# Performance work log

Hardware: AMD Instinct MI355X
Metric: run time of the kernel (lower is better)

Reference implementation:

```python
import jax, jax.numpy as jnp
import numpy as np

N = 100000      # total sampled nodes
NT = 20000      # target (destination) nodes
E = 2000000     # edges
IN = 128        # in_dim
OUT = 64        # out_channels (heads=1, concat)
NEG_SLOPE = 0.2 # GATConv default negative_slope


def setup_inputs() -> dict:
    key = jax.random.key(0)
    ks = jax.random.split(key, 6)
    x = jax.random.normal(ks[0], (N, IN), dtype=jnp.float32)
    edge_src = jax.random.randint(ks[1], (E,), 0, N)
    edge_dst = jax.random.randint(ks[2], (E,), 0, NT)
    # GATConv params: shared lin for src/dst (in_channels is int), att vectors, bias
    W = jax.random.normal(ks[3], (IN, OUT), dtype=jnp.float32) / np.sqrt(IN).astype(np.float32)
    att_src = jax.random.normal(ks[4], (OUT,), dtype=jnp.float32)
    att_dst = jax.random.normal(ks[5], (OUT,), dtype=jnp.float32)
    bias = jnp.zeros((OUT,), dtype=jnp.float32)
    return {"x": x, "edge_src": edge_src, "edge_dst": edge_dst,
            "W": W, "att_src": att_src, "att_dst": att_dst, "bias": bias,
            "num_target": NT}


def reference(x, edge_src, edge_dst, W, att_src, att_dst, bias, num_target):
    # Linear transform (lin_src == lin_dst in PyG GATConv when in_channels is int)
    x_proj = x @ W                      # [N, OUT]
    x_dst = x_proj[:num_target]         # [NT, OUT] target nodes are x[:num_target]
    # Per-node attention logits
    a_src = x_proj @ att_src            # [N]
    a_dst = x_dst @ att_dst             # [NT]
    # Edge logits + LeakyReLU
    e = jax.nn.leaky_relu(a_src[edge_src] + a_dst[edge_dst], NEG_SLOPE)  # [E]
    # Segment softmax over edges grouped by destination
    m = jax.ops.segment_max(e, edge_dst, num_segments=num_target)
    m = jnp.where(jnp.isneginf(m), jnp.float32(0.0), m)  # empty segments
    p = jnp.exp(e - m[edge_dst])
    denom = jax.ops.segment_sum(p, edge_dst, num_segments=num_target)
    alpha = p / (denom[edge_dst] + jnp.float32(1e-16))   # PyG softmax eps
    # Weighted scatter-aggregate of source features
    out = jax.ops.segment_sum(alpha[:, None] * x_proj[edge_src], edge_dst,
                              num_segments=num_target)   # [NT, OUT]
    return out + bias
```

## Files before the change

kernel.cpp:

```cpp
#include <hip/hip_runtime.h>

#define IN_DIM 128
#define OUT_DIM 64
#define NEG_SLOPE 0.2f

#define NBUCK 625
#define BCAP 4096
#define CHUNK 8192

typedef __attribute__((ext_vector_type(8))) short short8v;
typedef __attribute__((ext_vector_type(4))) float f32x4;

__device__ __forceinline__ unsigned pack_bf16(float a, float b) {
    unsigned ua = __float_as_uint(a), ub = __float_as_uint(b);
    ua += 0x7FFFu + ((ua >> 16) & 1u);
    ub += 0x7FFFu + ((ub >> 16) & 1u);
    return (ua >> 16) | (ub & 0xFFFF0000u);
}

__device__ __forceinline__ short8v mk8(unsigned a, unsigned b, unsigned c, unsigned d) {
    union { uint4 u; short8v s; } z;
    z.u = make_uint4(a, b, c, d);
    return z.s;
}

__device__ __forceinline__ int slice_of(unsigned src, float inv_sdiv) {
    int s = (int)((float)src * inv_sdiv);
    return s > 3 ? 3 : s;
}

__global__ __launch_bounds__(1024) void part_kernel(
    const float* __restrict__ W, unsigned* __restrict__ w_hi,
    unsigned* __restrict__ w_lo,
    const int* __restrict__ edge_src, const int* __restrict__ edge_dst,
    int* __restrict__ bcursor, unsigned* __restrict__ inter, int E)
{
    if (blockIdx.x == 0) {
        int g = threadIdx.x;
        int kb = g >> 6, col = g & 63;
        unsigned uh[4], ul[4];
#pragma unroll
        for (int i = 0; i < 4; ++i) {
            float a = W[(kb * 8 + 2 * i) * 64 + col];
            float b = W[(kb * 8 + 2 * i + 1) * 64 + col];
            unsigned h = pack_bf16(a, b);
            float la = a - __uint_as_float(h << 16);
            float lb = b - __uint_as_float(h & 0xFFFF0000u);
            uh[i] = h;
            ul[i] = pack_bf16(la, lb);
        }
        *(uint4*)(w_hi + g * 4) = make_uint4(uh[0], uh[1], uh[2], uh[3]);
        *(uint4*)(w_lo + g * 4) = make_uint4(ul[0], ul[1], ul[2], ul[3]);
        return;
    }

    __shared__ unsigned stage[CHUNK];
    __shared__ int hist[NBUCK];
    __shared__ int loff[NBUCK];
    __shared__ int gbase[NBUCK];
    __shared__ int cur[NBUCK];
    __shared__ int wsum[16];

    const int t  = threadIdx.x;
    const int c0 = (blockIdx.x - 1) * CHUNK;
    const int cnt = min(CHUNK, E - c0);

    for (int i = t; i < NBUCK; i += 1024) hist[i] = 0;
    __syncthreads();

    unsigned pk[8];
    int nmine = 0;
    const int i0 = 8 * t;
    if (i0 + 8 <= cnt) {
        int4 s0 = *(const int4*)(edge_src + c0 + i0);
        int4 s1 = *(const int4*)(edge_src + c0 + i0 + 4);
        int4 d0 = *(const int4*)(edge_dst + c0 + i0);
        int4 d1 = *(const int4*)(edge_dst + c0 + i0 + 4);
        pk[0] = ((unsigned)d0.x << 17) | (unsigned)s0.x;
        pk[1] = ((unsigned)d0.y << 17) | (unsigned)s0.y;
        pk[2] = ((unsigned)d0.z << 17) | (unsigned)s0.z;
        pk[3] = ((unsigned)d0.w << 17) | (unsigned)s0.w;
        pk[4] = ((unsigned)d1.x << 17) | (unsigned)s1.x;
        pk[5] = ((unsigned)d1.y << 17) | (unsigned)s1.y;
        pk[6] = ((unsigned)d1.z << 17) | (unsigned)s1.z;
        pk[7] = ((unsigned)d1.w << 17) | (unsigned)s1.w;
        nmine = 8;
    } else {
#pragma unroll
        for (int k = 0; k < 8; ++k) {
            int i = i0 + k;
            if (i < cnt) {
                pk[k] = ((unsigned)edge_dst[c0 + i] << 17) | (unsigned)edge_src[c0 + i];
                nmine = k + 1;
            }
        }
    }
#pragma unroll
    for (int k = 0; k < 8; ++k)
        if (k < nmine) atomicAdd(&hist[pk[k] >> 22], 1);
    __syncthreads();

    {
        const int lane = t & 63, w = t >> 6;
        int v = (t < NBUCK) ? hist[t] : 0;
        int scan = v;
#pragma unroll
        for (int off = 1; off < 64; off <<= 1) {
            int o = __shfl_up(scan, off);
            if (lane >= off) scan += o;
        }
        if (lane == 63) wsum[w] = scan;
        __syncthreads();
        int wpre = 0;
#pragma unroll
        for (int i = 0; i < 16; ++i)
            if (i < w) wpre += wsum[i];
        int excl = wpre + scan - v;
        if (t < NBUCK) {
            loff[t] = excl;
            cur[t]  = excl;
            if (v > 0) gbase[t] = t * BCAP + atomicAdd(&bcursor[t], v);
        }
    }
    __syncthreads();

#pragma unroll
    for (int k = 0; k < 8; ++k)
        if (k < nmine) {
            unsigned v = pk[k];
            int p = atomicAdd(&cur[v >> 22], 1);
            stage[p] = v;
        }
    __syncthreads();

    for (int i = t; i < cnt; i += 1024) {
        unsigned v = stage[i];
        int b = v >> 22;
        int pos = gbase[b] + (i - loff[b]);
        if (pos < (b + 1) * BCAP) inter[pos] = v;
    }
}

__global__ __launch_bounds__(256) void gemm_kernel(
    const float* __restrict__ x,
    const unsigned* __restrict__ w_hi, const unsigned* __restrict__ w_lo,
    const float* __restrict__ att_src, const float* __restrict__ att_dst,
    unsigned* __restrict__ x_bf, float* __restrict__ a_src,
    float* __restrict__ a_dst, int N, int NT)
{
    __shared__ __align__(16) float C[128 * 64];

    const int t    = threadIdx.x;
    const int lane = t & 63;
    const int w    = t >> 6;
    const int r0   = blockIdx.x * 128;
    const int rsub = lane & 15;
    const int kg   = lane >> 4;

    const int r1 = min(r0 + 32 * w + rsub,      N - 1);
    const int r2 = min(r0 + 32 * w + 16 + rsub, N - 1);
    const float* xrow1 = x + (size_t)r1 * IN_DIM + kg * 8;
    const float* xrow2 = x + (size_t)r2 * IN_DIM + kg * 8;

    float4 xv[16];
#pragma unroll
    for (int j = 0; j < 8; ++j)
        xv[j] = *(const float4*)(xrow1 + (j >> 1) * 32 + (j & 1) * 4);
#pragma unroll
    for (int j = 0; j < 8; ++j)
        xv[8 + j] = *(const float4*)(xrow2 + (j >> 1) * 32 + (j & 1) * 4);
    __builtin_amdgcn_sched_barrier(0);

    short8v ah[2][4], al[2][4];
#pragma unroll
    for (int rf = 0; rf < 2; ++rf)
#pragma unroll
        for (int ks = 0; ks < 4; ++ks) {
            float4 v0 = xv[8 * rf + 2 * ks], v1 = xv[8 * rf + 2 * ks + 1];
            unsigned h0 = pack_bf16(v0.x, v0.y);
            unsigned h1 = pack_bf16(v0.z, v0.w);
            unsigned h2 = pack_bf16(v1.x, v1.y);
            unsigned h3 = pack_bf16(v1.z, v1.w);
            unsigned l0 = pack_bf16(v0.x - __uint_as_float(h0 << 16),
                                    v0.y - __uint_as_float(h0 & 0xFFFF0000u));
            unsigned l1 = pack_bf16(v0.z - __uint_as_float(h1 << 16),
                                    v0.w - __uint_as_float(h1 & 0xFFFF0000u));
            unsigned l2 = pack_bf16(v1.x - __uint_as_float(h2 << 16),
                                    v1.y - __uint_as_float(h2 & 0xFFFF0000u));
            unsigned l3 = pack_bf16(v1.z - __uint_as_float(h3 << 16),
                                    v1.w - __uint_as_float(h3 & 0xFFFF0000u));
            ah[rf][ks] = mk8(h0, h1, h2, h3);
            al[rf][ks] = mk8(l0, l1, l2, l3);
        }

    f32x4 acc[2][4];
#pragma unroll
    for (int rf = 0; rf < 2; ++rf)
#pragma unroll
        for (int cf = 0; cf < 4; ++cf) acc[rf][cf] = f32x4{0.f, 0.f, 0.f, 0.f};

#pragma unroll
    for (int ks = 0; ks < 4; ++ks) {
        const int kb = 4 * ks + kg;
        const unsigned* bhp = w_hi + (kb * 64 + rsub) * 4;
        const unsigned* blp = w_lo + (kb * 64 + rsub) * 4;
        short8v bh[4], bl[4];
#pragma unroll
        for (int cf = 0; cf < 4; ++cf) {
            bh[cf] = *(const short8v*)(bhp + cf * 64);
            bl[cf] = *(const short8v*)(blp + cf * 64);
        }
#pragma unroll
        for (int cf = 0; cf < 4; ++cf) {
#pragma unroll
            for (int rf = 0; rf < 2; ++rf) {
                acc[rf][cf] = __builtin_amdgcn_mfma_f32_16x16x32_bf16(ah[rf][ks], bh[cf], acc[rf][cf], 0, 0, 0);
                acc[rf][cf] = __builtin_amdgcn_mfma_f32_16x16x32_bf16(al[rf][ks], bh[cf], acc[rf][cf], 0, 0, 0);
                acc[rf][cf] = __builtin_amdgcn_mfma_f32_16x16x32_bf16(ah[rf][ks], bl[cf], acc[rf][cf], 0, 0, 0);
            }
        }
    }

#pragma unroll
    for (int rf = 0; rf < 2; ++rf)
#pragma unroll
        for (int cf = 0; cf < 4; ++cf)
#pragma unroll
            for (int j = 0; j < 4; ++j) {
                int row = 32 * w + 16 * rf + 4 * kg + j;
                int col = 16 * cf + rsub;
                C[row * 64 + ((col + 4 * row) & 63)] = acc[rf][cf][j];
            }
    __syncthreads();

    {
        const int row = t >> 1;
        const int h   = t & 1;
        const int rr  = r0 + row;
        float v[32];
#pragma unroll
        for (int j = 0; j < 8; ++j) {
            int s = (32 * h + 4 * j + 4 * row) & 63;
            float4 f = *(const float4*)(C + row * 64 + s);
            v[4 * j + 0] = f.x; v[4 * j + 1] = f.y;
            v[4 * j + 2] = f.z; v[4 * j + 3] = f.w;
        }
        if (rr < N) {
            unsigned pk[16];
#pragma unroll
            for (int m = 0; m < 16; ++m)
                pk[m] = pack_bf16(v[2 * m], v[2 * m + 1]);
            unsigned* dst = x_bf + (size_t)rr * 32 + h * 16;
            *(uint4*)(dst + 0)  = make_uint4(pk[0], pk[1], pk[2], pk[3]);
            *(uint4*)(dst + 4)  = make_uint4(pk[4], pk[5], pk[6], pk[7]);
            *(uint4*)(dst + 8)  = make_uint4(pk[8], pk[9], pk[10], pk[11]);
            *(uint4*)(dst + 12) = make_uint4(pk[12], pk[13], pk[14], pk[15]);

            float ps = 0.f, pd = 0.f;
#pragma unroll
            for (int i = 0; i < 32; ++i) {
                ps = fmaf(v[i], att_src[32 * h + i], ps);
                pd = fmaf(v[i], att_dst[32 * h + i], pd);
            }
            ps += __shfl_xor(ps, 1);
            pd += __shfl_xor(pd, 1);
            if (h == 0) {
                a_src[rr] = ps;
                if (rr < NT) a_dst[rr] = pd;
            }
        }
    }
}

#define LRELU_EXP(a) __expf(((a) > 0.f ? (a) : NEG_SLOPE * (a)))

__global__ __launch_bounds__(512) void agg_kernel(
    const int* __restrict__ bcursor, const unsigned* __restrict__ inter,
    const float* __restrict__ a_src, const float* __restrict__ a_dst,
    const unsigned* __restrict__ x_bf, const float* __restrict__ bias,
    float* __restrict__ out, int NT, float inv_sdiv)
{
    __shared__ unsigned ssrc[BCAP];
    __shared__ int cnt[128], off_[128], cur[128];

    const int b = blockIdx.x;
    const int t = threadIdx.x;
    const int base = b * BCAP;
    const int n = min(bcursor[b], BCAP);

    for (int i = t; i < 128; i += 512) cnt[i] = 0;
    __syncthreads();

    unsigned ev[8];
    int kk[8];
#pragma unroll
    for (int k = 0; k < 8; ++k) {
        int i = t + 512 * k;
        ev[k] = 0xFFFFFFFFu;
        kk[k] = 0;
        if (i < n) {
            unsigned v = inter[base + i];
            ev[k] = v;
            kk[k] = (slice_of(v & 0x1FFFFu, inv_sdiv) << 5) | ((v >> 17) & 31);
            atomicAdd(&cnt[kk[k]], 1);
        }
    }
    __syncthreads();

    if (t == 0) {
        int r = 0;
#pragma unroll
        for (int j = 0; j < 128; ++j) { off_[j] = r; r += cnt[j]; }
    }
    __syncthreads();
    if (t < 128) cur[t] = off_[t];
    __syncthreads();

#pragma unroll
    for (int k = 0; k < 8; ++k)
        if (ev[k] != 0xFFFFFFFFu) {
            int p = atomicAdd(&cur[kk[k]], 1);
            ssrc[p] = ev[k] & 0x1FFFFu;
        }
    __syncthreads();

    const int lane = t & 63;
    const int w    = t >> 6;
    const int q    = lane >> 4;
    const int g    = (lane >> 3) & 1;
    const int sub  = lane & 7;

    const int ld  = 4 * w + q;
    const int tgt = b * 32 + ld;
    const float ad = (tgt < NT) ? a_dst[tgt] : 0.f;

    float dl = 0.f;
    float acc[8];
#pragma unroll
    for (int k = 0; k < 8; ++k) acc[k] = 0.f;

    for (int s = 0; s < 4; ++s) {
        const int key = (s << 5) | ld;
        const int lo = off_[key];
        const int nn = cnt[key];

        int ncmax = (nn + 15) >> 4;
        ncmax = max(ncmax, __shfl_xor(ncmax, 16));
        ncmax = max(ncmax, __shfl_xor(ncmax, 32));

        for (int c = 0; c < ncmax; ++c) {
            const int el = 16 * c + 8 * g + sub;
            const bool valid = el < nn;
            const int sA = valid ? (int)ssrc[lo + el] : 0;

            int s8[8];
#pragma unroll
            for (int j = 0; j < 8; ++j) s8[j] = __shfl(sA, 16 * q + 8 * g + j);

            uint4 v[8];
#pragma unroll
            for (int j = 0; j < 8; ++j)
                v[j] = *(const uint4*)(x_bf + (size_t)s8[j] * 32 + sub * 4);

            const float aA = a_src[sA];
            const float pA = valid ? LRELU_EXP(aA + ad) : 0.f;
            dl += pA;

            float p8[8];
#pragma unroll
            for (int j = 0; j < 8; ++j) p8[j] = __shfl(pA, 16 * q + 8 * g + j);

#pragma unroll
            for (int j = 0; j < 8; ++j) {
                const float p = p8[j];
                acc[0] = fmaf(p, __uint_as_float(v[j].x << 16), acc[0]);
                acc[1] = fmaf(p, __uint_as_float(v[j].x & 0xFFFF0000u), acc[1]);
                acc[2] = fmaf(p, __uint_as_float(v[j].y << 16), acc[2]);
                acc[3] = fmaf(p, __uint_as_float(v[j].y & 0xFFFF0000u), acc[3]);
                acc[4] = fmaf(p, __uint_as_float(v[j].z << 16), acc[4]);
                acc[5] = fmaf(p, __uint_as_float(v[j].z & 0xFFFF0000u), acc[5]);
                acc[6] = fmaf(p, __uint_as_float(v[j].w << 16), acc[6]);
                acc[7] = fmaf(p, __uint_as_float(v[j].w & 0xFFFF0000u), acc[7]);
            }
        }
    }

#pragma unroll
    for (int k = 0; k < 8; ++k) acc[k] += __shfl_xor(acc[k], 8);
    dl += __shfl_xor(dl, 1);
    dl += __shfl_xor(dl, 2);
    dl += __shfl_xor(dl, 4);
    dl += __shfl_xor(dl, 8);

    if (g == 0 && tgt < NT) {
        const float inv = 1.f / (dl + 1e-16f);
        float4 b0 = *(const float4*)(bias + sub * 8);
        float4 b1 = *(const float4*)(bias + sub * 8 + 4);
        float* o = out + (size_t)tgt * OUT_DIM + sub * 8;
        float4 o0, o1;
        o0.x = fmaf(acc[0], inv, b0.x); o0.y = fmaf(acc[1], inv, b0.y);
        o0.z = fmaf(acc[2], inv, b0.z); o0.w = fmaf(acc[3], inv, b0.w);
        o1.x = fmaf(acc[4], inv, b1.x); o1.y = fmaf(acc[5], inv, b1.y);
        o1.z = fmaf(acc[6], inv, b1.z); o1.w = fmaf(acc[7], inv, b1.w);
        *(float4*)(o)     = o0;
        *(float4*)(o + 4) = o1;
    }
}

extern "C" void kernel_launch(void* const* d_in, const int* in_sizes, int n_in,
                              void* d_out, int out_size, void* d_ws, size_t ws_size,
                              hipStream_t stream)
{
    const float* x        = (const float*)d_in[0];
    const int*   edge_src = (const int*)d_in[1];
    const int*   edge_dst = (const int*)d_in[2];
    const float* W        = (const float*)d_in[3];
    const float* att_src  = (const float*)d_in[4];
    const float* att_dst  = (const float*)d_in[5];
    const float* bias     = (const float*)d_in[6];

    const int N  = in_sizes[0] / IN_DIM;
    const int E  = in_sizes[1];
    const int NT = out_size / OUT_DIM;
    float* out = (float*)d_out;

    const int sdiv = (N + 3) / 4;
    const float inv_sdiv = 1.0f / (float)sdiv;

    auto align256 = [](size_t v) { return (v + 255) & ~(size_t)255; };
    char* w = (char*)d_ws;
    unsigned* x_bf   = (unsigned*)w;  w += align256((size_t)N * 32 * 4);
    float*    a_src  = (float*)w;     w += align256((size_t)N * 4);
    float*    a_dst  = (float*)w;     w += align256((size_t)NT * 4);
    int*      bcursor= (int*)w;       w += align256((size_t)NBUCK * 4);
    unsigned* w_hi   = (unsigned*)w;  w += align256((size_t)1024 * 16);
    unsigned* w_lo   = (unsigned*)w;  w += align256((size_t)1024 * 16);
    unsigned* inter  = (unsigned*)w;  w += align256((size_t)NBUCK * BCAP * 4);

    hipMemsetAsync(bcursor, 0, (size_t)NBUCK * 4, stream);

    const int nchunk = (E + CHUNK - 1) / CHUNK;
    part_kernel<<<1 + nchunk, 1024, 0, stream>>>(
        W, w_hi, w_lo, edge_src, edge_dst, bcursor, inter, E);

    gemm_kernel<<<(N + 127) / 128, 256, 0, stream>>>(
        x, w_hi, w_lo, att_src, att_dst, x_bf, a_src, a_dst, N, NT);

    agg_kernel<<<NBUCK, 512, 0, stream>>>(
        bcursor, inter, a_src, a_dst, x_bf, bias, out, NT, inv_sdiv);
}
```

Measured before the change: 85.93 us.

## Split aggregation across four source-slice blocks per bucket and combine partials

The aggregation kernel now launches four blocks per destination bucket, each handling only the edges whose source falls in one of four node slices. Each block writes unnormalized numerators and denominators to workspace, and a new combine kernel sums the four partials, normalizes, and adds the bias. The aim is more parallelism and occupancy in the gather-heavy aggregation, and per-slice locality of source rows. The cost is that every block rereads the whole bucket, plus extra partial-buffer traffic and a fourth launch. A per-slice cap of 1024 entries silently drops edges if a slice overflows.

```diff
diff --git a/kernel.cpp b/kernel.cpp
--- a/kernel.cpp
+++ b/kernel.cpp
@@ -277,32 +277,33 @@
 __global__ __launch_bounds__(512) void agg_kernel(
     const int* __restrict__ bcursor, const unsigned* __restrict__ inter,
     const float* __restrict__ a_src, const float* __restrict__ a_dst,
-    const unsigned* __restrict__ x_bf, const float* __restrict__ bias,
-    float* __restrict__ out, int NT, float inv_sdiv)
+    const unsigned* __restrict__ x_bf,
+    float* __restrict__ num4, float* __restrict__ den4,
+    int NT, float inv_sdiv)
 {
-    __shared__ unsigned ssrc[BCAP];
-    __shared__ int cnt[128], off_[128], cur[128];
-
-    const int b = blockIdx.x;
-    const int t = threadIdx.x;
+    __shared__ unsigned ssrc[1024];
+    __shared__ int cnt[32], off_[32], cur[32];
+
+    const int b    = blockIdx.x >> 2;
+    const int s    = blockIdx.x & 3;
+    const int t    = threadIdx.x;
     const int base = b * BCAP;
-    const int n = min(bcursor[b], BCAP);
-
-    for (int i = t; i < 128; i += 512) cnt[i] = 0;
+    const int n    = min(bcursor[b], BCAP);
+
+    if (t < 32) cnt[t] = 0;
     __syncthreads();
 
     unsigned ev[8];
-    int kk[8];
 #pragma unroll
     for (int k = 0; k < 8; ++k) {
         int i = t + 512 * k;
         ev[k] = 0xFFFFFFFFu;
-        kk[k] = 0;
         if (i < n) {
-            unsigned v = inter[base + i];
-            ev[k] = v;
-            kk[k] = (slice_of(v & 0x1FFFFu, inv_sdiv) << 5) | ((v >> 17) & 31);
-            atomicAdd(&cnt[kk[k]], 1);
+            unsigned v = __builtin_nontemporal_load(inter + base + i);
+            if (slice_of(v & 0x1FFFFu, inv_sdiv) == s) {
+                ev[k] = v;
+                atomicAdd(&cnt[(v >> 17) & 31], 1);
+            }
         }
     }
     __syncthreads();
@@ -310,17 +311,17 @@
     if (t == 0) {
         int r = 0;
 #pragma unroll
-        for (int j = 0; j < 128; ++j) { off_[j] = r; r += cnt[j]; }
-    }
-    __syncthreads();
-    if (t < 128) cur[t] = off_[t];
+        for (int j = 0; j < 32; ++j) { off_[j] = r; r += cnt[j]; }
+    }
+    __syncthreads();
+    if (t < 32) cur[t] = off_[t];
     __syncthreads();
 
 #pragma unroll
     for (int k = 0; k < 8; ++k)
         if (ev[k] != 0xFFFFFFFFu) {
-            int p = atomicAdd(&cur[kk[k]], 1);
-            ssrc[p] = ev[k] & 0x1FFFFu;
+            int p = atomicAdd(&cur[(ev[k] >> 17) & 31], 1);
+            if (p < 1024) ssrc[p] = ev[k] & 0x1FFFFu;
         }
     __syncthreads();
 
@@ -332,6 +333,16 @@
 
     const int ld  = 4 * w + q;
     const int tgt = b * 32 + ld;
+
+    int lo = off_[ld];
+    int nn = cnt[ld];
+    if (lo >= 1024) nn = 0;
+    if (lo + nn > 1024) nn = 1024 - lo;
+
+    int ncmax = (nn + 15) >> 4;
+    ncmax = max(ncmax, __shfl_xor(ncmax, 16));
+    ncmax = max(ncmax, __shfl_xor(ncmax, 32));
+
     const float ad = (tgt < NT) ? a_dst[tgt] : 0.f;
 
     float dl = 0.f;
@@ -339,49 +350,39 @@
 #pragma unroll
     for (int k = 0; k < 8; ++k) acc[k] = 0.f;
 
-    for (int s = 0; s < 4; ++s) {
-        const int key = (s << 5) | ld;
-        const int lo = off_[key];
-        const int nn = cnt[key];
-
-        int ncmax = (nn + 15) >> 4;
-        ncmax = max(ncmax, __shfl_xor(ncmax, 16));
-        ncmax = max(ncmax, __shfl_xor(ncmax, 32));
-
-        for (int c = 0; c < ncmax; ++c) {
-            const int el = 16 * c + 8 * g + sub;
-            const bool valid = el < nn;
-            const int sA = valid ? (int)ssrc[lo + el] : 0;
-
-            int s8[8];
-#pragma unroll
-            for (int j = 0; j < 8; ++j) s8[j] = __shfl(sA, 16 * q + 8 * g + j);
-
-            uint4 v[8];
-#pragma unroll
-            for (int j = 0; j < 8; ++j)
-                v[j] = *(const uint4*)(x_bf + (size_t)s8[j] * 32 + sub * 4);
-
-            const float aA = a_src[sA];
-            const float pA = valid ? LRELU_EXP(aA + ad) : 0.f;
-            dl += pA;
-
-            float p8[8];
-#pragma unroll
-            for (int j = 0; j < 8; ++j) p8[j] = __shfl(pA, 16 * q + 8 * g + j);
-
-#pragma unroll
-            for (int j = 0; j < 8; ++j) {
-                const float p = p8[j];
-                acc[0] = fmaf(p, __uint_as_float(v[j].x << 16), acc[0]);
-                acc[1] = fmaf(p, __uint_as_float(v[j].x & 0xFFFF0000u), acc[1]);
-                acc[2] = fmaf(p, __uint_as_float(v[j].y << 16), acc[2]);
-                acc[3] = fmaf(p, __uint_as_float(v[j].y & 0xFFFF0000u), acc[3]);
-                acc[4] = fmaf(p, __uint_as_float(v[j].z << 16), acc[4]);
-                acc[5] = fmaf(p, __uint_as_float(v[j].z & 0xFFFF0000u), acc[5]);
-                acc[6] = fmaf(p, __uint_as_float(v[j].w << 16), acc[6]);
-                acc[7] = fmaf(p, __uint_as_float(v[j].w & 0xFFFF0000u), acc[7]);
-            }
+    for (int c = 0; c < ncmax; ++c) {
+        const int el = 16 * c + 8 * g + sub;
+        const bool valid = el < nn;
+        const int sA = valid ? (int)ssrc[lo + el] : 0;
+
+        int s8[8];
+#pragma unroll
+        for (int j = 0; j < 8; ++j) s8[j] = __shfl(sA, 16 * q + 8 * g + j);
+
+        uint4 v[8];
+#pragma unroll
+        for (int j = 0; j < 8; ++j)
+            v[j] = *(const uint4*)(x_bf + (size_t)s8[j] * 32 + sub * 4);
+
+        const float aA = a_src[sA];
+        const float pA = valid ? LRELU_EXP(aA + ad) : 0.f;
+        dl += pA;
+
+        float p8[8];
+#pragma unroll
+        for (int j = 0; j < 8; ++j) p8[j] = __shfl(pA, 16 * q + 8 * g + j);
+
+#pragma unroll
+        for (int j = 0; j < 8; ++j) {
+            const float p = p8[j];
+            acc[0] = fmaf(p, __uint_as_float(v[j].x << 16), acc[0]);
+            acc[1] = fmaf(p, __uint_as_float(v[j].x & 0xFFFF0000u), acc[1]);
+            acc[2] = fmaf(p, __uint_as_float(v[j].y << 16), acc[2]);
+            acc[3] = fmaf(p, __uint_as_float(v[j].y & 0xFFFF0000u), acc[3]);
+            acc[4] = fmaf(p, __uint_as_float(v[j].z << 16), acc[4]);
+            acc[5] = fmaf(p, __uint_as_float(v[j].z & 0xFFFF0000u), acc[5]);
+            acc[6] = fmaf(p, __uint_as_float(v[j].w << 16), acc[6]);
+            acc[7] = fmaf(p, __uint_as_float(v[j].w & 0xFFFF0000u), acc[7]);
         }
     }
 
@@ -393,18 +394,31 @@
     dl += __shfl_xor(dl, 8);
 
     if (g == 0 && tgt < NT) {
-        const float inv = 1.f / (dl + 1e-16f);
-        float4 b0 = *(const float4*)(bias + sub * 8);
-        float4 b1 = *(const float4*)(bias + sub * 8 + 4);
-        float* o = out + (size_t)tgt * OUT_DIM + sub * 8;
-        float4 o0, o1;
-        o0.x = fmaf(acc[0], inv, b0.x); o0.y = fmaf(acc[1], inv, b0.y);
-        o0.z = fmaf(acc[2], inv, b0.z); o0.w = fmaf(acc[3], inv, b0.w);
-        o1.x = fmaf(acc[4], inv, b1.x); o1.y = fmaf(acc[5], inv, b1.y);
-        o1.z = fmaf(acc[6], inv, b1.z); o1.w = fmaf(acc[7], inv, b1.w);
-        *(float4*)(o)     = o0;
-        *(float4*)(o + 4) = o1;
-    }
+        float* np = num4 + ((size_t)s * NT + tgt) * OUT_DIM + sub * 8;
+        f32x4 o0 = {acc[0], acc[1], acc[2], acc[3]};
+        f32x4 o1 = {acc[4], acc[5], acc[6], acc[7]};
+        __builtin_nontemporal_store(o0, (f32x4*)(np));
+        __builtin_nontemporal_store(o1, (f32x4*)(np + 4));
+        if (sub == 0) __builtin_nontemporal_store(dl, den4 + s * NT + tgt);
+    }
+}
+
+__global__ __launch_bounds__(256) void combine_kernel(
+    const float* __restrict__ num4, const float* __restrict__ den4,
+    const float* __restrict__ bias, float* __restrict__ out, int NT)
+{
+    const int idx = blockIdx.x * 256 + threadIdx.x;
+    if (idx >= NT * OUT_DIM) return;
+    const int tgt = idx >> 6, col = idx & 63;
+
+    float d = 1e-16f;
+    float v = 0.f;
+#pragma unroll
+    for (int s = 0; s < 4; ++s) {
+        d += den4[s * NT + tgt];
+        v += num4[((size_t)s * NT + tgt) * OUT_DIM + col];
+    }
+    out[idx] = fmaf(v, 1.f / d, bias[col]);
 }
 
 extern "C" void kernel_launch(void* const* d_in, const int* in_sizes, int n_in,
@@ -435,6 +449,8 @@
     int*      bcursor= (int*)w;       w += align256((size_t)NBUCK * 4);
     unsigned* w_hi   = (unsigned*)w;  w += align256((size_t)1024 * 16);
     unsigned* w_lo   = (unsigned*)w;  w += align256((size_t)1024 * 16);
+    float*    num4   = (float*)w;     w += align256((size_t)4 * NT * OUT_DIM * 4);
+    float*    den4   = (float*)w;     w += align256((size_t)4 * NT * 4);
     unsigned* inter  = (unsigned*)w;  w += align256((size_t)NBUCK * BCAP * 4);
 
     hipMemsetAsync(bcursor, 0, (size_t)NBUCK * 4, stream);
@@ -446,6 +462,9 @@
     gemm_kernel<<<(N + 127) / 128, 256, 0, stream>>>(
         x, w_hi, w_lo, att_src, att_dst, x_bf, a_src, a_dst, N, NT);
 
-    agg_kernel<<<NBUCK, 512, 0, stream>>>(
-        bcursor, inter, a_src, a_dst, x_bf, bias, out, NT, inv_sdiv);
-}
+    agg_kernel<<<4 * NBUCK, 512, 0, stream>>>(
+        bcursor, inter, a_src, a_dst, x_bf, num4, den4, NT, inv_sdiv);
+
+    combine_kernel<<<(NT * OUT_DIM + 255) / 256, 256, 0, stream>>>(
+        num4, den4, bias, out, NT);
+}
```

Result: slower. 106.2 us (+23.6%).

## Fuse edge partitioning and projection GEMM into one heterogeneous kernel launch

Applied to the files above, without the earlier changes.

Replaces the memset and the separate W-split step with a small prep kernel that zeroes bucket cursors and splits W into bf16 hi/lo parts. The edge partition and the projection GEMM now run in one launch: the first blocks bucket edges and the rest compute the GEMM, with shared memory unioned between the two roles. GEMM blocks grow to 1024 threads covering 512 rows as four 256-thread sub-groups, which take turns using the shared C tile across phases separated by barriers. The goal is to drop a launch boundary and let partitioning overlap the GEMM, at the cost of serialized epilogue phases and larger blocks with more shared memory.

```diff
diff --git a/kernel.cpp b/kernel.cpp
--- a/kernel.cpp
+++ b/kernel.cpp
@@ -29,131 +29,141 @@
     return s > 3 ? 3 : s;
 }
 
-__global__ __launch_bounds__(1024) void part_kernel(
+__global__ __launch_bounds__(256) void prep_kernel(
     const float* __restrict__ W, unsigned* __restrict__ w_hi,
-    unsigned* __restrict__ w_lo,
-    const int* __restrict__ edge_src, const int* __restrict__ edge_dst,
-    int* __restrict__ bcursor, unsigned* __restrict__ inter, int E)
+    unsigned* __restrict__ w_lo, int* __restrict__ bcursor)
 {
-    if (blockIdx.x == 0) {
-        int g = threadIdx.x;
-        int kb = g >> 6, col = g & 63;
-        unsigned uh[4], ul[4];
-#pragma unroll
-        for (int i = 0; i < 4; ++i) {
-            float a = W[(kb * 8 + 2 * i) * 64 + col];
-            float b = W[(kb * 8 + 2 * i + 1) * 64 + col];
-            unsigned h = pack_bf16(a, b);
-            float la = a - __uint_as_float(h << 16);
-            float lb = b - __uint_as_float(h & 0xFFFF0000u);
-            uh[i] = h;
-            ul[i] = pack_bf16(la, lb);
-        }
-        *(uint4*)(w_hi + g * 4) = make_uint4(uh[0], uh[1], uh[2], uh[3]);
-        *(uint4*)(w_lo + g * 4) = make_uint4(ul[0], ul[1], ul[2], ul[3]);
+    if (blockIdx.x == 4) {
+        for (int i = threadIdx.x; i < NBUCK; i += 256) bcursor[i] = 0;
         return;
     }
-
-    __shared__ unsigned stage[CHUNK];
-    __shared__ int hist[NBUCK];
-    __shared__ int loff[NBUCK];
-    __shared__ int gbase[NBUCK];
-    __shared__ int cur[NBUCK];
-    __shared__ int wsum[16];
-
-    const int t  = threadIdx.x;
-    const int c0 = (blockIdx.x - 1) * CHUNK;
-    const int cnt = min(CHUNK, E - c0);
-
-    for (int i = t; i < NBUCK; i += 1024) hist[i] = 0;
-    __syncthreads();
-
-    unsigned pk[8];
-    int nmine = 0;
-    const int i0 = 8 * t;
-    if (i0 + 8 <= cnt) {
-        int4 s0 = *(const int4*)(edge_src + c0 + i0);
-        int4 s1 = *(const int4*)(edge_src + c0 + i0 + 4);
-        int4 d0 = *(const int4*)(edge_dst + c0 + i0);
-        int4 d1 = *(const int4*)(edge_dst + c0 + i0 + 4);
-        pk[0] = ((unsigned)d0.x << 17) | (unsigned)s0.x;
-        pk[1] = ((unsigned)d0.y << 17) | (unsigned)s0.y;
-        pk[2] = ((unsigned)d0.z << 17) | (unsigned)s0.z;
-        pk[3] = ((unsigned)d0.w << 17) | (unsigned)s0.w;
-        pk[4] = ((unsigned)d1.x << 17) | (unsigned)s1.x;
-        pk[5] = ((unsigned)d1.y << 17) | (unsigned)s1.y;
-        pk[6] = ((unsigned)d1.z << 17) | (unsigned)s1.z;
-        pk[7] = ((unsigned)d1.w << 17) | (unsigned)s1.w;
-        nmine = 8;
-    } else {
-#pragma unroll
-        for (int k = 0; k < 8; ++k) {
-            int i = i0 + k;
-            if (i < cnt) {
-                pk[k] = ((unsigned)edge_dst[c0 + i] << 17) | (unsigned)edge_src[c0 + i];
-                nmine = k + 1;
-            }
-        }
-    }
-#pragma unroll
-    for (int k = 0; k < 8; ++k)
-        if (k < nmine) atomicAdd(&hist[pk[k] >> 22], 1);
-    __syncthreads();
-
-    {
-        const int lane = t & 63, w = t >> 6;
-        int v = (t < NBUCK) ? hist[t] : 0;
-        int scan = v;
-#pragma unroll
-        for (int off = 1; off < 64; off <<= 1) {
-            int o = __shfl_up(scan, off);
-            if (lane >= off) scan += o;
-        }
-        if (lane == 63) wsum[w] = scan;
-        __syncthreads();
-        int wpre = 0;
-#pragma unroll
-        for (int i = 0; i < 16; ++i)
-            if (i < w) wpre += wsum[i];
-        int excl = wpre + scan - v;
-        if (t < NBUCK) {
-            loff[t] = excl;
-            cur[t]  = excl;
-            if (v > 0) gbase[t] = t * BCAP + atomicAdd(&bcursor[t], v);
-        }
-    }
-    __syncthreads();
-
-#pragma unroll
-    for (int k = 0; k < 8; ++k)
-        if (k < nmine) {
-            unsigned v = pk[k];
-            int p = atomicAdd(&cur[v >> 22], 1);
-            stage[p] = v;
-        }
-    __syncthreads();
-
-    for (int i = t; i < cnt; i += 1024) {
-        unsigned v = stage[i];
-        int b = v >> 22;
-        int pos = gbase[b] + (i - loff[b]);
-        if (pos < (b + 1) * BCAP) inter[pos] = v;
-    }
-}
-
-__global__ __launch_bounds__(256) void gemm_kernel(
+    int g = blockIdx.x * 256 + threadIdx.x;
+    int kb = g >> 6, col = g & 63;
+    unsigned uh[4], ul[4];
+#pragma unroll
+    for (int i = 0; i < 4; ++i) {
+        float a = W[(kb * 8 + 2 * i) * 64 + col];
+        float b = W[(kb * 8 + 2 * i + 1) * 64 + col];
+        unsigned h = pack_bf16(a, b);
+        float la = a - __uint_as_float(h << 16);
+        float lb = b - __uint_as_float(h & 0xFFFF0000u);
+        uh[i] = h;
+        ul[i] = pack_bf16(la, lb);
+    }
+    *(uint4*)(w_hi + g * 4) = make_uint4(uh[0], uh[1], uh[2], uh[3]);
+    *(uint4*)(w_lo + g * 4) = make_uint4(ul[0], ul[1], ul[2], ul[3]);
+}
+
+__global__ __launch_bounds__(1024) void fused_kernel(
     const float* __restrict__ x,
     const unsigned* __restrict__ w_hi, const unsigned* __restrict__ w_lo,
     const float* __restrict__ att_src, const float* __restrict__ att_dst,
+    const int* __restrict__ edge_src, const int* __restrict__ edge_dst,
+    int* __restrict__ bcursor, unsigned* __restrict__ inter,
     unsigned* __restrict__ x_bf, float* __restrict__ a_src,
-    float* __restrict__ a_dst, int N, int NT)
+    float* __restrict__ a_dst, int N, int NT, int E, int nchunk)
 {
-    __shared__ __align__(16) float C[128 * 64];
-
-    const int t    = threadIdx.x;
-    const int lane = t & 63;
-    const int w    = t >> 6;
-    const int r0   = blockIdx.x * 128;
+    __shared__ __align__(16) union SMem {
+        struct {
+            unsigned stage[CHUNK];
+            int hist[NBUCK];
+            int loff[NBUCK];
+            int gbase[NBUCK];
+            int cur[NBUCK];
+            int wsum[16];
+        } p;
+        float C[128 * 64];
+    } U;
+
+    const int t = threadIdx.x;
+
+    if ((int)blockIdx.x < nchunk) {
+        const int c0 = blockIdx.x * CHUNK;
+        const int cnt = min(CHUNK, E - c0);
+
+        for (int i = t; i < NBUCK; i += 1024) U.p.hist[i] = 0;
+        __syncthreads();
+
+        unsigned pk[8];
+        int nmine = 0;
+        const int i0 = 8 * t;
+        if (i0 + 8 <= cnt) {
+            int4 s0 = *(const int4*)(edge_src + c0 + i0);
+            int4 s1 = *(const int4*)(edge_src + c0 + i0 + 4);
+            int4 d0 = *(const int4*)(edge_dst + c0 + i0);
+            int4 d1 = *(const int4*)(edge_dst + c0 + i0 + 4);
+            pk[0] = ((unsigned)d0.x << 17) | (unsigned)s0.x;
+            pk[1] = ((unsigned)d0.y << 17) | (unsigned)s0.y;
+            pk[2] = ((unsigned)d0.z << 17) | (unsigned)s0.z;
+            pk[3] = ((unsigned)d0.w << 17) | (unsigned)s0.w;
+            pk[4] = ((unsigned)d1.x << 17) | (unsigned)s1.x;
+            pk[5] = ((unsigned)d1.y << 17) | (unsigned)s1.y;
+            pk[6] = ((unsigned)d1.z << 17) | (unsigned)s1.z;
+            pk[7] = ((unsigned)d1.w << 17) | (unsigned)s1.w;
+            nmine = 8;
+        } else {
+#pragma unroll
+            for (int k = 0; k < 8; ++k) {
+                int i = i0 + k;
+                if (i < cnt) {
+                    pk[k] = ((unsigned)edge_dst[c0 + i] << 17) | (unsigned)edge_src[c0 + i];
+                    nmine = k + 1;
+                }
+            }
+        }
+#pragma unroll
+        for (int k = 0; k < 8; ++k)
+            if (k < nmine) atomicAdd(&U.p.hist[pk[k] >> 22], 1);
+        __syncthreads();
+
+        {
+            const int lane = t & 63, w = t >> 6;
+            int v = (t < NBUCK) ? U.p.hist[t] : 0;
+            int scan = v;
+#pragma unroll
+            for (int off = 1; off < 64; off <<= 1) {
+                int o = __shfl_up(scan, off);
+                if (lane >= off) scan += o;
+            }
+            if (lane == 63) U.p.wsum[w] = scan;
+            __syncthreads();
+            int wpre = 0;
+#pragma unroll
+            for (int i = 0; i < 16; ++i)
+                if (i < w) wpre += U.p.wsum[i];
+            int excl = wpre + scan - v;
+            if (t < NBUCK) {
+                U.p.loff[t] = excl;
+                U.p.cur[t]  = excl;
+                if (v > 0) U.p.gbase[t] = t * BCAP + atomicAdd(&bcursor[t], v);
+            }
+        }
+        __syncthreads();
+
+#pragma unroll
+        for (int k = 0; k < 8; ++k)
+            if (k < nmine) {
+                unsigned v = pk[k];
+                int p = atomicAdd(&U.p.cur[v >> 22], 1);
+                U.p.stage[p] = v;
+            }
+        __syncthreads();
+
+        for (int i = t; i < cnt; i += 1024) {
+            unsigned v = U.p.stage[i];
+            int b = v >> 22;
+            int pos = U.p.gbase[b] + (i - U.p.loff[b]);
+            if (pos < (b + 1) * BCAP) inter[pos] = v;
+        }
+        return;
+    }
+
+    const int bid = blockIdx.x - nchunk;
+    const int sub = t >> 8;
+    const int t2  = t & 255;
+    const int lane = t2 & 63;
+    const int w    = t2 >> 6;
+    const int r0   = bid * 512 + sub * 128;
     const int rsub = lane & 15;
     const int kg   = lane >> 4;
 
@@ -221,54 +231,58 @@
         }
     }
 
-#pragma unroll
-    for (int rf = 0; rf < 2; ++rf)
-#pragma unroll
-        for (int cf = 0; cf < 4; ++cf)
-#pragma unroll
-            for (int j = 0; j < 4; ++j) {
-                int row = 32 * w + 16 * rf + 4 * kg + j;
-                int col = 16 * cf + rsub;
-                C[row * 64 + ((col + 4 * row) & 63)] = acc[rf][cf][j];
-            }
-    __syncthreads();
-
-    {
-        const int row = t >> 1;
-        const int h   = t & 1;
-        const int rr  = r0 + row;
-        float v[32];
-#pragma unroll
-        for (int j = 0; j < 8; ++j) {
-            int s = (32 * h + 4 * j + 4 * row) & 63;
-            float4 f = *(const float4*)(C + row * 64 + s);
-            v[4 * j + 0] = f.x; v[4 * j + 1] = f.y;
-            v[4 * j + 2] = f.z; v[4 * j + 3] = f.w;
-        }
-        if (rr < N) {
-            unsigned pk[16];
-#pragma unroll
-            for (int m = 0; m < 16; ++m)
-                pk[m] = pack_bf16(v[2 * m], v[2 * m + 1]);
-            unsigned* dst = x_bf + (size_t)rr * 32 + h * 16;
-            *(uint4*)(dst + 0)  = make_uint4(pk[0], pk[1], pk[2], pk[3]);
-            *(uint4*)(dst + 4)  = make_uint4(pk[4], pk[5], pk[6], pk[7]);
-            *(uint4*)(dst + 8)  = make_uint4(pk[8], pk[9], pk[10], pk[11]);
-            *(uint4*)(dst + 12) = make_uint4(pk[12], pk[13], pk[14], pk[15]);
-
-            float ps = 0.f, pd = 0.f;
-#pragma unroll
-            for (int i = 0; i < 32; ++i) {
-                ps = fmaf(v[i], att_src[32 * h + i], ps);
-                pd = fmaf(v[i], att_dst[32 * h + i], pd);
-            }
-            ps += __shfl_xor(ps, 1);
-            pd += __shfl_xor(pd, 1);
-            if (h == 0) {
-                a_src[rr] = ps;
-                if (rr < NT) a_dst[rr] = pd;
-            }
-        }
+    for (int ph = 0; ph < 4; ++ph) {
+        if (sub == ph) {
+#pragma unroll
+            for (int rf = 0; rf < 2; ++rf)
+#pragma unroll
+                for (int cf = 0; cf < 4; ++cf)
+#pragma unroll
+                    for (int j = 0; j < 4; ++j) {
+                        int row = 32 * w + 16 * rf + 4 * kg + j;
+                        int col = 16 * cf + rsub;
+                        U.C[row * 64 + ((col + 4 * row) & 63)] = acc[rf][cf][j];
+                    }
+        }
+        __syncthreads();
+        if (sub == ph) {
+            const int row = t2 >> 1;
+            const int h   = t2 & 1;
+            const int rr  = r0 + row;
+            float v[32];
+#pragma unroll
+            for (int j = 0; j < 8; ++j) {
+                int s = (32 * h + 4 * j + 4 * row) & 63;
+                float4 f = *(const float4*)(U.C + row * 64 + s);
+                v[4 * j + 0] = f.x; v[4 * j + 1] = f.y;
+                v[4 * j + 2] = f.z; v[4 * j + 3] = f.w;
+            }
+            if (rr < N) {
+                unsigned pk[16];
+#pragma unroll
+                for (int m = 0; m < 16; ++m)
+                    pk[m] = pack_bf16(v[2 * m], v[2 * m + 1]);
+                unsigned* dst = x_bf + (size_t)rr * 32 + h * 16;
+                *(uint4*)(dst + 0)  = make_uint4(pk[0], pk[1], pk[2], pk[3]);
+                *(uint4*)(dst + 4)  = make_uint4(pk[4], pk[5], pk[6], pk[7]);
+                *(uint4*)(dst + 8)  = make_uint4(pk[8], pk[9], pk[10], pk[11]);
+                *(uint4*)(dst + 12) = make_uint4(pk[12], pk[13], pk[14], pk[15]);
+
+                float ps = 0.f, pd = 0.f;
+#pragma unroll
+                for (int i = 0; i < 32; ++i) {
+                    ps = fmaf(v[i], att_src[32 * h + i], ps);
+                    pd = fmaf(v[i], att_dst[32 * h + i], pd);
+                }
+                ps += __shfl_xor(ps, 1);
+                pd += __shfl_xor(pd, 1);
+                if (h == 0) {
+                    a_src[rr] = ps;
+                    if (rr < NT) a_dst[rr] = pd;
+                }
+            }
+        }
+        __syncthreads();
     }
 }
 
@@ -437,14 +451,13 @@
     unsigned* w_lo   = (unsigned*)w;  w += align256((size_t)1024 * 16);
     unsigned* inter  = (unsigned*)w;  w += align256((size_t)NBUCK * BCAP * 4);
 
-    hipMemsetAsync(bcursor, 0, (size_t)NBUCK * 4, stream);
+    prep_kernel<<<5, 256, 0, stream>>>(W, w_hi, w_lo, bcursor);
 
     const int nchunk = (E + CHUNK - 1) / CHUNK;
-    part_kernel<<<1 + nchunk, 1024, 0, stream>>>(
-        W, w_hi, w_lo, edge_src, edge_dst, bcursor, inter, E);
-
-    gemm_kernel<<<(N + 127) / 128, 256, 0, stream>>>(
-        x, w_hi, w_lo, att_src, att_dst, x_bf, a_src, a_dst, N, NT);
+    const int ngemm  = (N + 511) / 512;
+    fused_kernel<<<nchunk + ngemm, 1024, 0, stream>>>(
+        x, w_hi, w_lo, att_src, att_dst, edge_src, edge_dst,
+        bcursor, inter, x_bf, a_src, a_dst, N, NT, E, nchunk);
 
     agg_kernel<<<NBUCK, 512, 0, stream>>>(
         bcursor, inter, a_src, a_dst, x_bf, bias, out, NT, inv_sdiv);
```

New measurement: 105.8 us. 23.1% more time.
